# Kernel optimization log

Hardware: AMD Instinct MI355X
Metric: run time of the kernel (lower is better)

## Reference

```python
import jax, jax.numpy as jnp
import numpy as np

B, S, HID = 2, 2048, 2048
NH, DN, DR, DV, RANK = 16, 128, 64, 128, 512
DQK = DN + DR
SCALE = DQK ** -0.5
EPS = 1e-5


def _rope(x, theta):
    # x: [..., d] with d even; theta broadcastable to [..., d//2] (angle per pair)
    x1, x2 = x[..., 0::2], x[..., 1::2]
    c, s = jnp.cos(theta), jnp.sin(theta)
    return jnp.stack([x1 * c - x2 * s, x1 * s + x2 * c], axis=-1).reshape(x.shape)


def _layernorm(x, gamma, beta):
    mu = jnp.mean(x, axis=-1, keepdims=True)
    var = jnp.var(x, axis=-1, keepdims=True)
    return (x - mu) * jax.lax.rsqrt(var + EPS) * gamma + beta


def setup_inputs() -> dict:
    key = jax.random.key(0)
    ks = jax.random.split(key, 8)
    def xavier(k, fan_in, fan_out, gain=1.0):
        lim = gain * np.sqrt(6.0 / (fan_in + fan_out))
        return jax.random.uniform(k, (fan_in, fan_out), jnp.float32, -lim, lim)
    return {
        "hidden_states": jax.random.normal(ks[0], (B, S, HID), jnp.float32),
        "freqs_cis": jax.random.uniform(ks[1], (S, DR // 2), jnp.float32) * 2.0 * np.pi,
        "Wq": xavier(ks[2], HID, NH * DQK),                      # q_proj (stored [in,out])
        "Wkv_a": xavier(ks[3], HID, RANK + DR),                  # kv_proj_a
        "kv_gamma": jnp.ones((RANK,), jnp.float32),              # kv_norm
        "kv_beta": jnp.zeros((RANK,), jnp.float32),
        "Wkv_b": xavier(ks[4], RANK, NH * (DN + DV)),            # kv_proj_b
        "Wout": xavier(ks[5], NH * DV, HID, gain=1.0 / np.sqrt(2.0)),  # out_proj
    }


def reference(hidden_states, freqs_cis, Wq, Wkv_a, kv_gamma, kv_beta, Wkv_b, Wout):
    b, s, _ = hidden_states.shape
    max_len = freqs_cis.shape[0]
    pos = jnp.arange(s) % max_len                      # [s], position_ids=None path
    theta = freqs_cis[pos]                             # [s, DR//2]

    # Q projection, split nope/rope, partial RoPE
    q = (hidden_states @ Wq).reshape(b, s, NH, DQK)
    q_nope, q_rope = q[..., :DN], q[..., DN:]
    q_rope = _rope(q_rope, theta[None, :, None, :])    # [b,s,nh,DR]

    # Low-rank KV: compressed latent + shared rope key
    kv = hidden_states @ Wkv_a                         # [b,s,RANK+DR]
    kv_c, k_rope = kv[..., :RANK], kv[..., RANK:]
    k_rope = _rope(k_rope, theta[None, :, :])          # [b,s,DR]
    kv_c = _layernorm(kv_c, kv_gamma, kv_beta)
    kvb = (kv_c @ Wkv_b).reshape(b, s, NH, DN + DV)
    k_nope, v = kvb[..., :DN], kvb[..., DN:]
    k = jnp.concatenate(
        [k_nope, jnp.broadcast_to(k_rope[:, :, None, :], (b, s, NH, DR))], axis=-1)

    q = jnp.concatenate([q_nope, q_rope], axis=-1)     # [b,s,nh,DQK]
    scores = jnp.einsum('bthd,bshd->btsh', q, k) * SCALE
    weights = jax.nn.softmax(scores.astype(jnp.float32), axis=2).astype(q.dtype)
    attn = jnp.einsum('btsh,bshd->bthd', weights, v).reshape(b, s, NH * DV)
    return attn @ Wout
```

## Files before the change

kernel.cpp:

```cpp
#include <hip/hip_runtime.h>

#define BATCH 2
#define SEQ   2048
#define HID   2048
#define NH    16
#define DN    128
#define DR    64
#define DV    128
#define RANK  512
#define DQK   192
#define NQ    (NH*DQK)
#define NQKV  3712
#define NKVB  (NH*(DN+DV))
#define NTOK  (BATCH*SEQ)
#define SCALE_F 0.07216878364870323f
#define SCALE_LOG2E 0.10411754831420211f

typedef __bf16 bf16x8 __attribute__((ext_vector_type(8)));
typedef float  f32x4  __attribute__((ext_vector_type(4)));
typedef unsigned int u32x4 __attribute__((ext_vector_type(4)));
typedef unsigned short u16;
typedef unsigned short u16x4 __attribute__((ext_vector_type(4)));

__device__ __forceinline__ float b2f(u16 h) {
    unsigned int u = ((unsigned int)h) << 16;
    float f; __builtin_memcpy(&f, &u, 4); return f;
}
__device__ __forceinline__ u16 f2b(float f) {
    unsigned int x; __builtin_memcpy(&x, &f, 4);
    unsigned int r = x + 0x7fffu + ((x >> 16) & 1u);
    return (u16)(r >> 16);
}
__device__ __forceinline__ bf16x8 lds_frag(const u16* p) {
    u32x4 v = *(const u32x4*)p;
    return __builtin_bit_cast(bf16x8, v);
}
__device__ __forceinline__ bf16x8 to_frag(u32x4 v) {
    return __builtin_bit_cast(bf16x8, v);
}
__device__ __forceinline__ f32x4 mfma16(bf16x8 a, bf16x8 b, f32x4 c) {
    return __builtin_amdgcn_mfma_f32_16x16x32_bf16(a, b, c, 0, 0, 0);
}
__device__ __forceinline__ void store_out(u16* p, float v) { *p = f2b(v); }
__device__ __forceinline__ void store_out(float* p, float v) { *p = v; }
__device__ __forceinline__ void gld_lds16(const u16* g, u16* l) {
    __builtin_amdgcn_global_load_lds(
        (const __attribute__((address_space(1))) unsigned int*)g,
        (__attribute__((address_space(3))) unsigned int*)l, 16, 0, 0);
}

__global__ __launch_bounds__(256) void prep_kernel(
        const float* __restrict__ hs_f, u16* __restrict__ hs,
        const float* __restrict__ Wq, const float* __restrict__ Wkva,
        const float* __restrict__ Wkvb, const float* __restrict__ Wout,
        u16* __restrict__ WqkvT, u16* __restrict__ WkvbT, u16* __restrict__ WoutT) {
    int tid = threadIdx.x;
    int bid = blockIdx.x;
    if (bid < 8192) {
        int i = bid * 256 + tid;
        f32x4 v = *(const f32x4*)(hs_f + (size_t)i * 4);
        u16 o[4];
        for (int k = 0; k < 4; k++) o[k] = f2b(v[k]);
        *(unsigned long long*)(hs + (size_t)i * 4) = *(unsigned long long*)o;
        return;
    }
    bid -= 8192;
    const float* in; u16* out; int R, C, tilesC;
    if (bid < 1536)      { in = Wq;   out = WqkvT;                       R = HID;  C = NQ;   tilesC = 48; }
    else if (bid < 1856) { bid -= 1536; in = Wkva; out = WqkvT + (size_t)NQ * HID; R = HID; C = 576; tilesC = 10; }
    else if (bid < 2368) { bid -= 1856; in = Wkvb; out = WkvbT;          R = RANK; C = NKVB; tilesC = 64; }
    else                 { bid -= 2368; in = Wout; out = WoutT;          R = HID;  C = HID;  tilesC = 32; }
    __shared__ unsigned int t32[64 * 65];
    int r0 = (bid / tilesC) * 64, c0 = (bid % tilesC) * 64;
    bool valid = (c0 < C);
    for (int i = 0; i < 4; i++) {
        int u = tid + i * 256;
        int rl = u >> 4, c4 = u & 15;
        f32x4 v = {0.f, 0.f, 0.f, 0.f};
        if (valid) v = *(const f32x4*)&in[(size_t)(r0 + rl) * C + c0 + c4 * 4];
        for (int j = 0; j < 4; j++)
            t32[(c4 * 4 + j) * 65 + rl] = f2b(v[j]);
    }
    __syncthreads();
    for (int i = 0; i < 2; i++) {
        int u = tid + i * 256;
        int cl = u >> 3, r8 = (u & 7) * 8;
        unsigned int w[8];
        for (int j = 0; j < 8; j++) w[j] = t32[cl * 65 + r8 + j];
        u32x4 pk;
        for (int j = 0; j < 4; j++) pk[j] = (w[2 * j] & 0xffffu) | (w[2 * j + 1] << 16);
        *(u32x4*)&out[(size_t)(c0 + cl) * R + r0 + r8] = pk;
    }
}

template <typename OutT>
__global__ __launch_bounds__(256) void gemm_bt(const u16* __restrict__ A,
                                               const u16* __restrict__ Bt,
                                               OutT* __restrict__ C,
                                               int K, int lda, int ldb, int ldc) {
    __shared__ u16 As[128 * 32];
    __shared__ u16 Bs[128 * 32];
    int tid = threadIdx.x, lane = tid & 63, w = tid >> 6;
    int wm = (w >> 1) * 64, wn = (w & 1) * 64;
    int g = lane >> 4, ln = lane & 15;
    int m0 = blockIdx.y * 128, n0 = blockIdx.x * 128;
    f32x4 acc[4][4] = {};
    for (int k0 = 0; k0 < K; k0 += 32) {
        for (int i = 0; i < 2; i++) {
            int ch = tid + i * 256;
            int row = ch >> 2, o = ch & 3;
            gld_lds16(&A[(size_t)(m0 + row) * lda + k0 + o * 8], &As[row * 32 + o * 8]);
            gld_lds16(&Bt[(size_t)(n0 + row) * ldb + k0 + o * 8], &Bs[row * 32 + o * 8]);
        }
        __syncthreads();
        bf16x8 af[4], bf[4];
        for (int i = 0; i < 4; i++) af[i] = lds_frag(&As[(wm + i * 16 + ln) * 32 + g * 8]);
        for (int j = 0; j < 4; j++) bf[j] = lds_frag(&Bs[(wn + j * 16 + ln) * 32 + g * 8]);
        for (int i = 0; i < 4; i++)
            for (int j = 0; j < 4; j++)
                acc[i][j] = mfma16(af[i], bf[j], acc[i][j]);
        __syncthreads();
    }
    for (int i = 0; i < 4; i++)
        for (int j = 0; j < 4; j++)
            for (int r = 0; r < 4; r++) {
                int m = m0 + wm + i * 16 + g * 4 + r;
                int n = n0 + wn + j * 16 + ln;
                store_out(&C[(size_t)m * ldc + n], acc[i][j][r]);
            }
}

__global__ void rope_q(u16* __restrict__ qkv, const float* __restrict__ freqs) {
    int token = blockIdx.x;
    int s = token & (SEQ - 1);
    int tid = threadIdx.x;
    for (int i = 0; i < 2; i++) {
        int idx = tid + i * 256;
        int hh = idx >> 5, p = idx & 31;
        float th = freqs[s * 32 + p];
        float c = __cosf(th), sn = __sinf(th);
        size_t off = (size_t)token * NQKV + hh * DQK + DN + 2 * p;
        float x1 = b2f(qkv[off]), x2 = b2f(qkv[off + 1]);
        qkv[off]     = f2b(x1 * c - x2 * sn);
        qkv[off + 1] = f2b(x1 * sn + x2 * c);
    }
}

__global__ void ln_kv(const u16* __restrict__ qkv, const float* __restrict__ gamma,
                      const float* __restrict__ beta, u16* __restrict__ kv_c) {
    int row = blockIdx.x, tid = threadIdx.x;
    size_t base = (size_t)row * NQKV + NQ;
    float x0 = b2f(qkv[base + tid]), x1 = b2f(qkv[base + 256 + tid]);
    float s = x0 + x1, q2 = x0 * x0 + x1 * x1;
    for (int o = 32; o > 0; o >>= 1) { s += __shfl_xor(s, o); q2 += __shfl_xor(q2, o); }
    __shared__ float sh[8];
    int lane = tid & 63, w = tid >> 6;
    if (lane == 0) { sh[w] = s; sh[4 + w] = q2; }
    __syncthreads();
    float S = sh[0] + sh[1] + sh[2] + sh[3];
    float Q2 = sh[4] + sh[5] + sh[6] + sh[7];
    float mu = S * (1.f / 512.f);
    float var = Q2 * (1.f / 512.f) - mu * mu;
    float rs = rsqrtf(var + 1e-5f);
    kv_c[(size_t)row * RANK + tid] =
        f2b((x0 - mu) * rs * gamma[tid] + beta[tid]);
    kv_c[(size_t)row * RANK + 256 + tid] =
        f2b((x1 - mu) * rs * gamma[256 + tid] + beta[256 + tid]);
}

__global__ void k_assemble(const u16* __restrict__ kvb, const u16* __restrict__ qkv,
                           const float* __restrict__ freqs, u16* __restrict__ Kf) {
    int token = blockIdx.x;
    int s = token & (SEQ - 1);
    int tid = threadIdx.x;
    __shared__ u16 roped[64];
    if (tid < 32) {
        int p = tid;
        float th = freqs[s * 32 + p];
        float c = __cosf(th), sn = __sinf(th);
        float x1 = b2f(qkv[(size_t)token * NQKV + NQ + RANK + 2 * p]);
        float x2 = b2f(qkv[(size_t)token * NQKV + NQ + RANK + 2 * p + 1]);
        roped[2 * p]     = f2b(x1 * c - x2 * sn);
        roped[2 * p + 1] = f2b(x1 * sn + x2 * c);
    }
    __syncthreads();
    {
        int hh = tid >> 4, d8 = (tid & 15) * 8;
        *(u32x4*)&Kf[(size_t)token * NQ + hh * DQK + d8] =
            *(const u32x4*)&kvb[(size_t)token * NKVB + hh * 256 + d8];
    }
    if (tid < 128) {
        int hh = tid >> 3, d8 = (tid & 7) * 8;
        *(u32x4*)&Kf[(size_t)token * NQ + hh * DQK + DN + d8] = *(u32x4*)&roped[d8];
    }
}

__global__ void v_transpose(const u16* __restrict__ kvb, u16* __restrict__ Vt) {
    __shared__ unsigned int t32[64 * 65];
    int st = blockIdx.x * 64, dt = blockIdx.y * 64;
    int b = blockIdx.z >> 4, h = blockIdx.z & 15;
    int tid = threadIdx.x;
    for (int i = 0; i < 2; i++) {
        int u = tid + i * 256;
        int sl = u >> 3, c8 = (u & 7) * 8;
        u32x4 v = *(const u32x4*)&kvb[((size_t)(b * SEQ + st + sl) * NH + h) * 256 + DN + dt + c8];
        for (int j = 0; j < 4; j++) {
            t32[(c8 + 2 * j) * 65 + sl]     = v[j] & 0xffffu;
            t32[(c8 + 2 * j + 1) * 65 + sl] = v[j] >> 16;
        }
    }
    __syncthreads();
    for (int i = 0; i < 2; i++) {
        int u = tid + i * 256;
        int dl = u >> 3, s8 = (u & 7) * 8;
        unsigned int w[8];
        for (int j = 0; j < 8; j++) w[j] = t32[dl * 65 + s8 + j];
        u32x4 pk;
        for (int j = 0; j < 4; j++) pk[j] = (w[2 * j] & 0xffffu) | (w[2 * j + 1] << 16);
        *(u32x4*)&Vt[((size_t)(b * NH + h) * DV + dt + dl) * SEQ + st + s8] = pk;
    }
}

#define KC    64
#define QTILE 64
#define PSTR 72
#define NIT  (SEQ / KC)
__global__ __launch_bounds__(256, 3) void attn_kernel(const u16* __restrict__ Q,
                                                      const u16* __restrict__ Kf,
                                                      const u16* __restrict__ Vt,
                                                      u16* __restrict__ O) {
    __shared__ u16 Ks[6 * 64 * 32];
    __shared__ u16 Vs[2 * 128 * 32];
    __shared__ u16 Ps[QTILE * PSTR];
    __shared__ float lsumLDS[2][QTILE];
    int tid = threadIdx.x, lane = tid & 63, w = tid >> 6;
    int w1 = w & 1;
    int w2 = w >> 1;
    int g = lane >> 4, ln = lane & 15;
    int qt = blockIdx.x, h = blockIdx.y, b = blockIdx.z;

    size_t qbase  = ((size_t)(b * SEQ + qt * QTILE)) * NQKV + h * DQK;
    size_t kbase0 = ((size_t)(b * SEQ) * NH + h) * DQK;
    size_t vbase  = (size_t)(b * NH + h) * DV * SEQ;

    bf16x8 bfq[2][6];
    for (int ni = 0; ni < 2; ni++)
        for (int kk = 0; kk < 6; kk++)
            bfq[ni][kk] = to_frag(*(const u32x4*)&Q[qbase +
                (size_t)(w1 * 32 + ni * 16 + ln) * NQKV + kk * 32 + g * 8]);

    int rswz = ((ln >> 1) & 3) << 4;
    int gb16 = g * 16;
    int kRd[2], vRd[4];
    for (int mi = 0; mi < 2; mi++) kRd[mi] = (w2 * 32 + mi * 16 + ln) * 64 + (gb16 ^ rswz);
    for (int ni = 0; ni < 4; ni++) vRd[ni] = (w2 * 64 + ni * 16 + ln) * 64 + (gb16 ^ rswz);
    int krow = tid >> 2, vrow = tid >> 1;
    int kswz = ((krow >> 1) & 3) << 4, vswz = ((vrow >> 1) & 3) << 4;
    int kWr  = krow * 64 + (((tid & 3) * 16) ^ kswz);
    int vWr0 = vrow * 64 + (((tid & 1) * 16) ^ vswz);
    int vWr1 = vrow * 64 + ((((tid & 1) + 2) * 16) ^ vswz);

    u32x4 kpre[6], vpre[4];
    {
        for (int i = 0; i < 6; i++) {
            int o = (tid & 3) + 4 * i;
            kpre[i] = *(const u32x4*)&Kf[kbase0 + (size_t)krow * NQ + o * 8];
        }
        for (int i = 0; i < 4; i++) {
            int o = (tid & 1) + 2 * i;
            vpre[i] = *(const u32x4*)&Vt[vbase + (size_t)vrow * SEQ + o * 8];
        }
    }
    f32x4 oacc[2][4] = {};
    float lpriv[2] = {0.f, 0.f};

    for (int kt = 0; kt < NIT; kt++) {
        for (int i = 0; i < 6; i++)
            *(u32x4*)((char*)Ks + i * 4096 + kWr) = kpre[i];
        for (int i = 0; i < 4; i++)
            *(u32x4*)((char*)Vs + (i >> 1) * 8192 + ((i & 1) ? vWr1 : vWr0)) = vpre[i];
        __syncthreads();
        if (kt + 1 < NIT) {
            size_t kb = kbase0 + (size_t)(kt + 1) * KC * NQ;
            for (int i = 0; i < 6; i++) {
                int o = (tid & 3) + 4 * i;
                kpre[i] = *(const u32x4*)&Kf[kb + (size_t)krow * NQ + o * 8];
            }
            int c0 = (kt + 1) * KC;
            for (int i = 0; i < 4; i++) {
                int o = (tid & 1) + 2 * i;
                vpre[i] = *(const u32x4*)&Vt[vbase + (size_t)vrow * SEQ + c0 + o * 8];
            }
        }
        f32x4 sacc[2][2] = {};
        for (int kk = 0; kk < 6; kk++) {
            bf16x8 af[2];
            for (int mi = 0; mi < 2; mi++)
                af[mi] = lds_frag((const u16*)((const char*)Ks + kk * 4096 + kRd[mi]));
            for (int mi = 0; mi < 2; mi++)
                for (int ni = 0; ni < 2; ni++)
                    sacc[mi][ni] = mfma16(af[mi], bfq[ni][kk], sacc[mi][ni]);
        }
        for (int mi = 0; mi < 2; mi++)
            for (int ni = 0; ni < 2; ni++) {
                float p0 = exp2f(sacc[mi][ni][0] * SCALE_LOG2E);
                float p1 = exp2f(sacc[mi][ni][1] * SCALE_LOG2E);
                float p2 = exp2f(sacc[mi][ni][2] * SCALE_LOG2E);
                float p3 = exp2f(sacc[mi][ni][3] * SCALE_LOG2E);
                lpriv[ni] += (p0 + p1) + (p2 + p3);
                unsigned int q0, q1;
                asm("v_cvt_pk_bf16_f32 %0, %1, %2" : "=v"(q0) : "v"(p0), "v"(p1));
                asm("v_cvt_pk_bf16_f32 %0, %1, %2" : "=v"(q1) : "v"(p2), "v"(p3));
                uint2 pk; pk.x = q0; pk.y = q1;
                *(uint2*)&Ps[(w1 * 32 + ni * 16 + ln) * PSTR + (w2 * 32 + mi * 16 + g * 4)] = pk;
            }
        __syncthreads();
        for (int kk = 0; kk < 2; kk++) {
            bf16x8 pa[2], vb[4];
            for (int mi = 0; mi < 2; mi++)
                pa[mi] = lds_frag(&Ps[(w1 * 32 + mi * 16 + ln) * PSTR + kk * 32 + g * 8]);
            for (int ni = 0; ni < 4; ni++)
                vb[ni] = lds_frag((const u16*)((const char*)Vs + kk * 8192 + vRd[ni]));
            for (int mi = 0; mi < 2; mi++)
                for (int ni = 0; ni < 4; ni++)
                    oacc[mi][ni] = mfma16(pa[mi], vb[ni], oacc[mi][ni]);
        }
        __syncthreads();
    }

    for (int ni = 0; ni < 2; ni++) {
        float v = lpriv[ni];
        v += __shfl_xor(v, 16);
        v += __shfl_xor(v, 32);
        if (g == 0) lsumLDS[w2][w1 * 32 + ni * 16 + ln] = v;
    }
    __syncthreads();
    for (int mi = 0; mi < 2; mi++)
        for (int ni = 0; ni < 4; ni++) {
            int d = w2 * 64 + ni * 16 + ln;
            for (int r = 0; r < 4; r++) {
                int row = w1 * 32 + mi * 16 + g * 4 + r;
                float l = lsumLDS[0][row] + lsumLDS[1][row];
                O[((size_t)(b * SEQ + qt * QTILE + row) * NH + h) * DV + d] =
                    f2b(oacc[mi][ni][r] / l);
            }
        }
}

extern "C" void kernel_launch(void* const* d_in, const int* in_sizes, int n_in,
                              void* d_out, int out_size, void* d_ws, size_t ws_size,
                              hipStream_t stream) {
    const float* hs_f  = (const float*)d_in[0];
    const float* freqs = (const float*)d_in[1];
    const float* Wq    = (const float*)d_in[2];
    const float* Wkva  = (const float*)d_in[3];
    const float* gamma = (const float*)d_in[4];
    const float* beta  = (const float*)d_in[5];
    const float* Wkvb  = (const float*)d_in[6];
    const float* Wout  = (const float*)d_in[7];
    float* outp = (float*)d_out;

    char* ws = (char*)d_ws;
    size_t off = 0;
    auto alloc = [&](size_t elems) -> u16* {
        u16* p = (u16*)(ws + off);
        off += ((elems * 2 + 255) / 256) * 256;
        return p;
    };
    u16* hs     = alloc((size_t)NTOK * HID);
    u16* WqkvT  = alloc((size_t)NQKV * HID);
    u16* WkvbT  = alloc((size_t)NKVB * RANK);
    u16* WoutT  = alloc((size_t)HID * HID);
    u16* qkv    = alloc((size_t)NTOK * NQKV);
    u16* kv_c   = alloc((size_t)NTOK * RANK);
    u16* kvb    = alloc((size_t)NTOK * NKVB);
    u16* Kf     = alloc((size_t)NTOK * NQ);
    u16* Vt     = alloc((size_t)BATCH * NH * DV * SEQ);
    u16* attn   = alloc((size_t)NTOK * NH * DV);
    (void)ws_size; (void)in_sizes; (void)n_in; (void)out_size;

    prep_kernel<<<8192 + 1536 + 320 + 512 + 1024, 256, 0, stream>>>(
        hs_f, hs, Wq, Wkva, Wkvb, Wout, WqkvT, WkvbT, WoutT);

    gemm_bt<<<dim3(NQKV / 128, NTOK / 128), 256, 0, stream>>>(hs, WqkvT, qkv, HID, HID, HID, NQKV);

    rope_q<<<NTOK, 256, 0, stream>>>(qkv, freqs);

    ln_kv<<<NTOK, 256, 0, stream>>>(qkv, gamma, beta, kv_c);

    gemm_bt<<<dim3(NKVB / 128, NTOK / 128), 256, 0, stream>>>(kv_c, WkvbT, kvb, RANK, RANK, RANK, NKVB);

    k_assemble<<<NTOK, 256, 0, stream>>>(kvb, qkv, freqs, Kf);

    v_transpose<<<dim3(SEQ / 64, DV / 64, BATCH * NH), 256, 0, stream>>>(kvb, Vt);

    attn_kernel<<<dim3(SEQ / QTILE, NH, BATCH), 256, 0, stream>>>(qkv, Kf, Vt, attn);

    gemm_bt<<<dim3(HID / 128, NTOK / 128), 256, 0, stream>>>(attn, WoutT, outp, HID, HID, HID, HID);
}
```

Baseline: 479.2 us.

## Pre-tile K and V into fragment-ready layout and read MFMA operands directly from global

k_assemble and v_transpose now write K and V in per-(batch,head,64-key-tile) blocks laid out so each MFMA fragment is a contiguous 16-byte load. The attention kernel drops the LDS staging of K/V and its register prefetch, reading fragments straight from global/L2. It double-buffers the P tile to remove one barrier per iteration, raises the occupancy hint to 4 blocks, and remaps block IDs so blocks sharing a head run close together. The cost is that every wave re-reads K/V from cache instead of sharing it through LDS, and there is no explicit prefetch left to hide memory latency.

```diff
diff --git a/kernel.cpp b/kernel.cpp
--- a/kernel.cpp
+++ b/kernel.cpp
@@ -171,6 +171,7 @@
 __global__ void k_assemble(const u16* __restrict__ kvb, const u16* __restrict__ qkv,
                            const float* __restrict__ freqs, u16* __restrict__ Kf) {
     int token = blockIdx.x;
+    int b = token >> 11;
     int s = token & (SEQ - 1);
     int tid = threadIdx.x;
     __shared__ u16 roped[64];
@@ -184,20 +185,25 @@
         roped[2 * p + 1] = f2b(x1 * sn + x2 * c);
     }
     __syncthreads();
+    int kt = s >> 6, r = s & 63;
     {
-        int hh = tid >> 4, d8 = (tid & 15) * 8;
-        *(u32x4*)&Kf[(size_t)token * NQ + hh * DQK + d8] =
-            *(const u32x4*)&kvb[(size_t)token * NKVB + hh * 256 + d8];
+        int hh = tid >> 4, c8 = (tid & 15) * 8;
+        size_t dst = ((size_t)(b * NH + hh) * 32 + kt) * 12288
+                   + (size_t)(c8 >> 5) * 2048 + r * 32 + (c8 & 31);
+        *(u32x4*)&Kf[dst] = *(const u32x4*)&kvb[(size_t)token * NKVB + hh * 256 + c8];
     }
     if (tid < 128) {
-        int hh = tid >> 3, d8 = (tid & 7) * 8;
-        *(u32x4*)&Kf[(size_t)token * NQ + hh * DQK + DN + d8] = *(u32x4*)&roped[d8];
+        int hh = tid >> 3, c8 = (tid & 7) * 8;
+        size_t dst = ((size_t)(b * NH + hh) * 32 + kt) * 12288
+                   + (size_t)(4 + (c8 >> 5)) * 2048 + r * 32 + (c8 & 31);
+        *(u32x4*)&Kf[dst] = *(u32x4*)&roped[c8];
     }
 }
 
 __global__ void v_transpose(const u16* __restrict__ kvb, u16* __restrict__ Vt) {
     __shared__ unsigned int t32[64 * 65];
-    int st = blockIdx.x * 64, dt = blockIdx.y * 64;
+    int bx = blockIdx.x;
+    int st = bx * 64, dt = blockIdx.y * 64;
     int b = blockIdx.z >> 4, h = blockIdx.z & 15;
     int tid = threadIdx.x;
     for (int i = 0; i < 2; i++) {
@@ -217,7 +223,9 @@
         for (int j = 0; j < 8; j++) w[j] = t32[dl * 65 + s8 + j];
         u32x4 pk;
         for (int j = 0; j < 4; j++) pk[j] = (w[2 * j] & 0xffffu) | (w[2 * j + 1] << 16);
-        *(u32x4*)&Vt[((size_t)(b * NH + h) * DV + dt + dl) * SEQ + st + s8] = pk;
+        size_t dst = ((size_t)(b * NH + h) * 32 + bx) * 8192
+                   + (size_t)(s8 >> 5) * 4096 + (size_t)(dt + dl) * 32 + (s8 & 31);
+        *(u32x4*)&Vt[dst] = pk;
     }
 }
 
@@ -225,23 +233,23 @@
 #define QTILE 64
 #define PSTR 72
 #define NIT  (SEQ / KC)
-__global__ __launch_bounds__(256, 3) void attn_kernel(const u16* __restrict__ Q,
+__global__ __launch_bounds__(256, 4) void attn_kernel(const u16* __restrict__ Q,
                                                       const u16* __restrict__ Kf,
                                                       const u16* __restrict__ Vt,
                                                       u16* __restrict__ O) {
-    __shared__ u16 Ks[6 * 64 * 32];
-    __shared__ u16 Vs[2 * 128 * 32];
-    __shared__ u16 Ps[QTILE * PSTR];
+    __shared__ u16 Ps[2][QTILE * PSTR];
     __shared__ float lsumLDS[2][QTILE];
     int tid = threadIdx.x, lane = tid & 63, w = tid >> 6;
     int w1 = w & 1;
     int w2 = w >> 1;
     int g = lane >> 4, ln = lane & 15;
-    int qt = blockIdx.x, h = blockIdx.y, b = blockIdx.z;
-
-    size_t qbase  = ((size_t)(b * SEQ + qt * QTILE)) * NQKV + h * DQK;
-    size_t kbase0 = ((size_t)(b * SEQ) * NH + h) * DQK;
-    size_t vbase  = (size_t)(b * NH + h) * DV * SEQ;
+    int bid = blockIdx.x;
+    int swz = ((bid & 7) << 7) | (bid >> 3);
+    int qt = swz & 31, h = (swz >> 5) & 15, b = swz >> 9;
+
+    size_t qbase = ((size_t)(b * SEQ + qt * QTILE)) * NQKV + h * DQK;
+    const u16* Kh = Kf + (size_t)(b * NH + h) * (32 * 12288);
+    const u16* Vh = Vt + (size_t)(b * NH + h) * (32 * 8192);
 
     bf16x8 bfq[2][6];
     for (int ni = 0; ni < 2; ni++)
@@ -249,58 +257,23 @@
             bfq[ni][kk] = to_frag(*(const u32x4*)&Q[qbase +
                 (size_t)(w1 * 32 + ni * 16 + ln) * NQKV + kk * 32 + g * 8]);
 
-    int rswz = ((ln >> 1) & 3) << 4;
-    int gb16 = g * 16;
-    int kRd[2], vRd[4];
-    for (int mi = 0; mi < 2; mi++) kRd[mi] = (w2 * 32 + mi * 16 + ln) * 64 + (gb16 ^ rswz);
-    for (int ni = 0; ni < 4; ni++) vRd[ni] = (w2 * 64 + ni * 16 + ln) * 64 + (gb16 ^ rswz);
-    int krow = tid >> 2, vrow = tid >> 1;
-    int kswz = ((krow >> 1) & 3) << 4, vswz = ((vrow >> 1) & 3) << 4;
-    int kWr  = krow * 64 + (((tid & 3) * 16) ^ kswz);
-    int vWr0 = vrow * 64 + (((tid & 1) * 16) ^ vswz);
-    int vWr1 = vrow * 64 + ((((tid & 1) + 2) * 16) ^ vswz);
-
-    u32x4 kpre[6], vpre[4];
-    {
-        for (int i = 0; i < 6; i++) {
-            int o = (tid & 3) + 4 * i;
-            kpre[i] = *(const u32x4*)&Kf[kbase0 + (size_t)krow * NQ + o * 8];
-        }
-        for (int i = 0; i < 4; i++) {
-            int o = (tid & 1) + 2 * i;
-            vpre[i] = *(const u32x4*)&Vt[vbase + (size_t)vrow * SEQ + o * 8];
-        }
-    }
     f32x4 oacc[2][4] = {};
     float lpriv[2] = {0.f, 0.f};
+    int arow = (w2 * 32 + ln) * 32 + g * 8;
+    int vrow = (w2 * 64 + ln) * 32 + g * 8;
 
     for (int kt = 0; kt < NIT; kt++) {
-        for (int i = 0; i < 6; i++)
-            *(u32x4*)((char*)Ks + i * 4096 + kWr) = kpre[i];
-        for (int i = 0; i < 4; i++)
-            *(u32x4*)((char*)Vs + (i >> 1) * 8192 + ((i & 1) ? vWr1 : vWr0)) = vpre[i];
-        __syncthreads();
-        if (kt + 1 < NIT) {
-            size_t kb = kbase0 + (size_t)(kt + 1) * KC * NQ;
-            for (int i = 0; i < 6; i++) {
-                int o = (tid & 3) + 4 * i;
-                kpre[i] = *(const u32x4*)&Kf[kb + (size_t)krow * NQ + o * 8];
-            }
-            int c0 = (kt + 1) * KC;
-            for (int i = 0; i < 4; i++) {
-                int o = (tid & 1) + 2 * i;
-                vpre[i] = *(const u32x4*)&Vt[vbase + (size_t)vrow * SEQ + c0 + o * 8];
-            }
-        }
+        const u16* kT = Kh + (size_t)kt * 12288;
         f32x4 sacc[2][2] = {};
         for (int kk = 0; kk < 6; kk++) {
             bf16x8 af[2];
             for (int mi = 0; mi < 2; mi++)
-                af[mi] = lds_frag((const u16*)((const char*)Ks + kk * 4096 + kRd[mi]));
+                af[mi] = to_frag(*(const u32x4*)&kT[kk * 2048 + mi * 512 + arow]);
             for (int mi = 0; mi < 2; mi++)
                 for (int ni = 0; ni < 2; ni++)
                     sacc[mi][ni] = mfma16(af[mi], bfq[ni][kk], sacc[mi][ni]);
         }
+        u16* Psb = Ps[kt & 1];
         for (int mi = 0; mi < 2; mi++)
             for (int ni = 0; ni < 2; ni++) {
                 float p0 = exp2f(sacc[mi][ni][0] * SCALE_LOG2E);
@@ -312,20 +285,20 @@
                 asm("v_cvt_pk_bf16_f32 %0, %1, %2" : "=v"(q0) : "v"(p0), "v"(p1));
                 asm("v_cvt_pk_bf16_f32 %0, %1, %2" : "=v"(q1) : "v"(p2), "v"(p3));
                 uint2 pk; pk.x = q0; pk.y = q1;
-                *(uint2*)&Ps[(w1 * 32 + ni * 16 + ln) * PSTR + (w2 * 32 + mi * 16 + g * 4)] = pk;
+                *(uint2*)&Psb[(w1 * 32 + ni * 16 + ln) * PSTR + (w2 * 32 + mi * 16 + g * 4)] = pk;
             }
         __syncthreads();
+        const u16* vT = Vh + (size_t)kt * 8192;
         for (int kk = 0; kk < 2; kk++) {
             bf16x8 pa[2], vb[4];
             for (int mi = 0; mi < 2; mi++)
-                pa[mi] = lds_frag(&Ps[(w1 * 32 + mi * 16 + ln) * PSTR + kk * 32 + g * 8]);
+                pa[mi] = lds_frag(&Psb[(w1 * 32 + mi * 16 + ln) * PSTR + kk * 32 + g * 8]);
             for (int ni = 0; ni < 4; ni++)
-                vb[ni] = lds_frag((const u16*)((const char*)Vs + kk * 8192 + vRd[ni]));
+                vb[ni] = to_frag(*(const u32x4*)&vT[kk * 4096 + ni * 512 + vrow]);
             for (int mi = 0; mi < 2; mi++)
                 for (int ni = 0; ni < 4; ni++)
                     oacc[mi][ni] = mfma16(pa[mi], vb[ni], oacc[mi][ni]);
         }
-        __syncthreads();
     }
 
     for (int ni = 0; ni < 2; ni++) {
@@ -394,7 +367,7 @@
 
     v_transpose<<<dim3(SEQ / 64, DV / 64, BATCH * NH), 256, 0, stream>>>(kvb, Vt);
 
-    attn_kernel<<<dim3(SEQ / QTILE, NH, BATCH), 256, 0, stream>>>(qkv, Kf, Vt, attn);
+    attn_kernel<<<1024, 256, 0, stream>>>(qkv, Kf, Vt, attn);
 
     gemm_bt<<<dim3(HID / 128, NTOK / 128), 256, 0, stream>>>(attn, WoutT, outp, HID, HID, HID, HID);
 }
```

After: 506.4 us. +5.7%, slower.
